# Kernel optimization log

Hardware: AMD Instinct MI355X
Metric: run time of the kernel (lower is better)

The kernel has to match this reference:

```python
import jax, jax.numpy as jnp
import numpy as np

S, B, D, H, L = 512, 512, 300, 256, 3

def setup_inputs() -> dict:
    key = jax.random.key(0)
    ks = jax.random.split(key, 9)
    sc = 0.02
    return {
        "x": jax.random.normal(ks[0], (S, B, D), dtype=jnp.float32),
        "fW_ih0": jax.random.normal(ks[1], (D, H), dtype=jnp.float32) * sc,
        "fW_ih": jax.random.normal(ks[2], (L - 1, H, H), dtype=jnp.float32) * sc,
        "fW_hh": jax.random.normal(ks[3], (L, H, H), dtype=jnp.float32) * sc,
        "fb": jnp.zeros((L, H), dtype=jnp.float32),
        "bW_ih0": jax.random.normal(ks[4], (D, H), dtype=jnp.float32) * sc,
        "bW_ih": jax.random.normal(ks[5], (L - 1, H, H), dtype=jnp.float32) * sc,
        "bW_hh": jax.random.normal(ks[6], (L, H, H), dtype=jnp.float32) * sc,
        "bb": jnp.zeros((L, H), dtype=jnp.float32),
    }

def _run_rnn(x, W_ih0, W_ih, W_hh, b):
    # x: [S, B, D]; stacked vanilla tanh RNN with L layers.
    batch = x.shape[1]
    h0 = jnp.zeros((L, batch, H), dtype=x.dtype)

    def step(h, x_t):  # h: [L, B, H], x_t: [B, D]
        inp = x_t
        new_h = []
        for l in range(L):
            Wih = W_ih0 if l == 0 else W_ih[l - 1]
            hl = jnp.tanh(inp @ Wih + h[l] @ W_hh[l] + b[l])
            new_h.append(hl)
            inp = hl
        return jnp.stack(new_h, axis=0), None

    h_final, _ = jax.lax.scan(step, h0, x)
    return h_final  # [L, B, H]

def reference(x, fW_ih0, fW_ih, fW_hh, fb, bW_ih0, bW_ih, bW_hh, bb):
    hf = _run_rnn(x, fW_ih0, fW_ih, fW_hh, fb)          # forward direction
    hb = _run_rnn(x[::-1], bW_ih0, bW_ih, bW_hh, bb)    # backward direction
    return jnp.concatenate((hf[-1], hb[-1]), axis=-1)   # [B, 2H]
```

## Files before the change

kernel.cpp:

```cpp
#include <hip/hip_runtime.h>
#include <cstdint>
#include <cstddef>


#define SEQ   512
#define BATCH 512
#define DIN   300
#define HDIM  256
#define NT    512
#define CH    64
#define NCH   (SEQ / CH)
#define NSLOT (NCH + 2)
#define TS    16
#define ZTILE 131072

typedef _Float16 f16x8 __attribute__((ext_vector_type(8)));
typedef __fp16   fp16x2 __attribute__((ext_vector_type(2)));
typedef float    f32x4 __attribute__((ext_vector_type(4)));

#define WIH0_E 0
#define WHH_E  163840
#define WIHN_E 557056
#define HC_BYTE   1638400
#define HB_BYTE   3211264
#define Z0_BYTE   (HB_BYTE + 67108864)
#define Z1_BYTE   (Z0_BYTE + 268435456)
#define Z2_BYTE   (Z1_BYTE + 67108864)
#define RING_E    8388608ull

static __device__ __forceinline__ uint16_t f16bits(_Float16 h) {
    union { _Float16 h; uint16_t u; } v; v.h = h; return v.u;
}
static __device__ __forceinline__ uint32_t pk2(float a, float b) {
    union { fp16x2 h; uint32_t u; } v; v.h = __builtin_amdgcn_cvt_pkrtz(a, b); return v.u;
}
static __device__ __forceinline__ int swz(int row, int col) {
    return (row * 256 + col) ^ ((row & 7) << 3);
}

static __device__ __forceinline__ void aload8(f16x8 r[8], const _Float16* p, size_t stepE) {
    const _Float16* p0 = p;
    const _Float16* p1 = p + stepE;
    const _Float16* p2 = p + 2 * stepE;
    const _Float16* p3 = p + 3 * stepE;
    const _Float16* p4 = p + 4 * stepE;
    const _Float16* p5 = p + 5 * stepE;
    const _Float16* p6 = p + 6 * stepE;
    const _Float16* p7 = p + 7 * stepE;
    asm volatile(
        "global_load_dwordx4 %0, %8, off\n\t"
        "global_load_dwordx4 %1, %9, off\n\t"
        "global_load_dwordx4 %2, %10, off\n\t"
        "global_load_dwordx4 %3, %11, off\n\t"
        "global_load_dwordx4 %4, %12, off\n\t"
        "global_load_dwordx4 %5, %13, off\n\t"
        "global_load_dwordx4 %6, %14, off\n\t"
        "global_load_dwordx4 %7, %15, off\n\t"
        "s_waitcnt vmcnt(0)"
        : "=&v"(r[0]), "=&v"(r[1]), "=&v"(r[2]), "=&v"(r[3]),
          "=&v"(r[4]), "=&v"(r[5]), "=&v"(r[6]), "=&v"(r[7])
        : "v"(p0), "v"(p1), "v"(p2), "v"(p3), "v"(p4), "v"(p5), "v"(p6), "v"(p7)
        : "memory");
}

__global__ void rnn_prep(const float* __restrict__ fW_ih0, const float* __restrict__ fW_ih,
                         const float* __restrict__ fW_hh,  const float* __restrict__ bW_ih0,
                         const float* __restrict__ bW_ih,  const float* __restrict__ bW_hh,
                         _Float16* __restrict__ wf)
{
    const int gid = blockIdx.x * 256 + threadIdx.x;
    const int d = gid / 51200;
    const int r = gid - d * 51200;
    const int lane = r & 63;
    const float* Wih0 = d ? bW_ih0 : fW_ih0;
    const float* Wih  = d ? bW_ih  : fW_ih;
    const float* Whh  = d ? bW_hh  : fW_hh;
    _Float16 vals[8];
    size_t dstE;
    if (r < 10240) {
        const int ck = r >> 6, ct = ck / 10, kt = ck - ct * 10;
        const int col = ct * 16 + (lane & 15);
        const int k0  = kt * 32 + (lane >> 4) * 8;
        #pragma unroll
        for (int e = 0; e < 8; ++e) {
            const int k = k0 + e;
            vals[e] = (k < 300) ? (_Float16)Wih0[(size_t)k * 256 + col] : (_Float16)0.f;
        }
        dstE = (size_t)WIH0_E + (size_t)d * 81920 + (size_t)r * 8;
    } else if (r < 34816) {
        const int rr = r - 10240, l = rr / 8192, r2 = rr - l * 8192;
        const int ck = r2 >> 6, ct = ck >> 3, kt = ck & 7;
        const int col = ct * 16 + (lane & 15);
        const int k0  = kt * 32 + (lane >> 4) * 8;
        #pragma unroll
        for (int e = 0; e < 8; ++e)
            vals[e] = (_Float16)Whh[((size_t)(l * 256 + k0 + e)) * 256 + col];
        dstE = (size_t)WHH_E + (size_t)(d * 3 + l) * 65536 + (size_t)r2 * 8;
    } else {
        const int rr = r - 34816, ln = rr / 8192, r2 = rr - ln * 8192;
        const int ck = r2 >> 6, ct = ck >> 3, kt = ck & 7;
        const int col = ct * 16 + (lane & 15);
        const int k0  = kt * 32 + (lane >> 4) * 8;
        #pragma unroll
        for (int e = 0; e < 8; ++e)
            vals[e] = (_Float16)Wih[((size_t)(ln * 256 + k0 + e)) * 256 + col];
        dstE = (size_t)WIHN_E + (size_t)(d * 2 + ln) * 65536 + (size_t)r2 * 8;
    }
    *(f16x8*)(wf + dstE) = *(const f16x8*)vals;
}

__global__ __attribute__((amdgpu_flat_work_group_size(NT, NT)))
void rnn_gemm0(const float* __restrict__ x, const _Float16* __restrict__ wih0,
               const float* __restrict__ fb, const float* __restrict__ bb,
               uint16_t* __restrict__ z0)
{
    __shared__ uint16_t Xl[2][16 * 332];
    const int tid = threadIdx.x, lane = tid & 63, w = tid >> 6;
    const int colw = lane & 15, rq = lane >> 4, rq8 = rq * 8;
    const int ct0 = w * 2;
    const int sg = blockIdx.x >> 5, rb = blockIdx.x & 31;
    const int b0 = rb * 16;
    const size_t chunk = ((size_t)(rb * 8 + w) * 64 + lane) * 8;

    int rs[5], cc2[5]; bool pv[5];
    #pragma unroll
    for (int b = 0; b < 5; ++b) {
        const int p = tid + b * NT;
        pv[b] = p < 2400;
        const int r = p / 150;
        rs[b] = r; cc2[b] = (p - r * 150) * 2;
    }

    float bv[2][2];
    #pragma unroll
    for (int dd = 0; dd < 2; ++dd)
        #pragma unroll
        for (int c = 0; c < 2; ++c)
            bv[dd][c] = (dd ? bb : fb)[(ct0 + c) * 16 + colw];

    for (int p = tid; p < 320; p += NT) {
        const int bu = p / 160, q = p - bu * 160;
        const int r = q / 10, cc = 300 + (q - r * 10) * 2;
        *(uint32_t*)&Xl[bu][r * 332 + cc] = 0;
    }
    {
        const float* xs = x + ((size_t)(sg * TS) * BATCH + b0) * DIN;
        #pragma unroll
        for (int b = 0; b < 5; ++b) if (pv[b]) {
            const float2 v = *(const float2*)(xs + (size_t)rs[b] * DIN + cc2[b]);
            *(uint32_t*)&Xl[0][rs[b] * 332 + cc2[b]] = pk2(v.x, v.y);
        }
    }
    __syncthreads();

    #pragma unroll 1
    for (int si = 0; si < TS; ++si) {
        const int s = sg * TS + si;
        const int buf = si & 1;
        const bool last = (si == TS - 1);

        {
            f32x4 a0 = (f32x4){bv[0][0], bv[0][0], bv[0][0], bv[0][0]};
            f32x4 a1 = (f32x4){bv[0][1], bv[0][1], bv[0][1], bv[0][1]};
            #pragma unroll
            for (int kt = 0; kt < 10; ++kt) {
                const f16x8 wv0 = *(const f16x8*)(wih0 + (((size_t)ct0 * 10 + kt) * 64 + lane) * 8);
                const f16x8 wv1 = *(const f16x8*)(wih0 + (((size_t)(ct0 + 1) * 10 + kt) * 64 + lane) * 8);
                const f16x8 a = *(const f16x8*)&Xl[buf][colw * 332 + kt * 32 + rq8];
                a0 = __builtin_amdgcn_mfma_f32_16x16x32_f16(a, wv0, a0, 0, 0, 0);
                a1 = __builtin_amdgcn_mfma_f32_16x16x32_f16(a, wv1, a1, 0, 0, 0);
            }
            uint4 sv;
            sv.x = pk2(a0[0], a0[1]); sv.y = pk2(a0[2], a0[3]);
            sv.z = pk2(a1[0], a1[1]); sv.w = pk2(a1[2], a1[3]);
            *(uint4*)(z0 + (size_t)s * ZTILE + chunk) = sv;
        }

        float2 xr[5];
        if (!last) {
            const float* xs = x + ((size_t)(s + 1) * BATCH + b0) * DIN;
            #pragma unroll
            for (int b = 0; b < 5; ++b) if (pv[b])
                xr[b] = *(const float2*)(xs + (size_t)rs[b] * DIN + cc2[b]);
        }

        f32x4 a0 = (f32x4){bv[1][0], bv[1][0], bv[1][0], bv[1][0]};
        f32x4 a1 = (f32x4){bv[1][1], bv[1][1], bv[1][1], bv[1][1]};
        #pragma unroll
        for (int kt = 0; kt < 10; ++kt) {
            const f16x8 wv0 = *(const f16x8*)(wih0 + 81920 + (((size_t)ct0 * 10 + kt) * 64 + lane) * 8);
            const f16x8 wv1 = *(const f16x8*)(wih0 + 81920 + (((size_t)(ct0 + 1) * 10 + kt) * 64 + lane) * 8);
            const f16x8 a = *(const f16x8*)&Xl[buf][colw * 332 + kt * 32 + rq8];
            a0 = __builtin_amdgcn_mfma_f32_16x16x32_f16(a, wv0, a0, 0, 0, 0);
            a1 = __builtin_amdgcn_mfma_f32_16x16x32_f16(a, wv1, a1, 0, 0, 0);
        }

        if (!last) {
            #pragma unroll
            for (int b = 0; b < 5; ++b) if (pv[b])
                *(uint32_t*)&Xl[buf ^ 1][rs[b] * 332 + cc2[b]] = pk2(xr[b].x, xr[b].y);
        }

        {
            uint4 sv;
            sv.x = pk2(a0[0], a0[1]); sv.y = pk2(a0[2], a0[3]);
            sv.z = pk2(a1[0], a1[1]); sv.w = pk2(a1[2], a1[3]);
            *(uint4*)(z0 + ((size_t)SEQ + (SEQ - 1 - s)) * ZTILE + chunk) = sv;
        }

        __builtin_amdgcn_sched_barrier(0);
        asm volatile("s_waitcnt lgkmcnt(0)" ::: "memory");
        __builtin_amdgcn_s_barrier();
        __builtin_amdgcn_sched_barrier(0);
    }
}

template<int L>
__device__ __forceinline__ void rec_run(const _Float16* whh_all, const _Float16* wihn_all,
                                        const uint16_t* zsrc, uint16_t* zdst,
                                        uint16_t* hcarry, const float* fb, const float* bb,
                                        float* out, int d, int i, int cs, uint16_t* Hb)
{
    const int tid = threadIdx.x, lane = tid & 63, w = tid >> 6;
    const int colw = lane & 15, rq = lane >> 4, rq8 = rq * 8;
    const int ct0 = w * 2;
    const int grow0 = i * 16;

    const _Float16* whh = whh_all + (size_t)(d * 3 + L) * 65536;
    f16x8 wh0[8], wh1[8];
    aload8(wh0, whh + ((size_t)ct0 * 8 * 64 + lane) * 8, 512);
    aload8(wh1, whh + ((size_t)(ct0 + 1) * 8 * 64 + lane) * 8, 512);
    f16x8 wn0[8], wn1[8];
    float bn0 = 0.f, bn1 = 0.f;
    if constexpr (L < 2) {
        const _Float16* wnx = wihn_all + (size_t)(d * 2 + L) * 65536;
        aload8(wn0, wnx + ((size_t)ct0 * 8 * 64 + lane) * 8, 512);
        aload8(wn1, wnx + ((size_t)(ct0 + 1) * 8 * 64 + lane) * 8, 512);
        const float* bnx = (d ? bb : fb) + (L + 1) * HDIM;
        bn0 = bnx[ct0 * 16 + colw];
        bn1 = bnx[(ct0 + 1) * 16 + colw];
    }

    for (int p = tid; p < 4096; p += NT) ((uint32_t*)Hb)[p] = 0;
    __syncthreads();
    if (cs > 0) {
        const uint16_t* hc = hcarry + (size_t)(d * 3 + L) * 131072;
        const int row = tid >> 5, c8 = (tid & 31) * 8;
        *(uint4*)&Hb[4096 + ((row * 256 + c8) ^ ((row & 7) << 3))] =
            *(const uint4*)(hc + (size_t)(grow0 + row) * 256 + c8);
    }
    __syncthreads();

    const size_t zoff = ((size_t)(i * 8 + w) * 64 + lane) * 8;

    uint4 zc = *(const uint4*)(zsrc + zoff);
    uint4 za = *(const uint4*)(zsrc + (size_t)ZTILE + zoff);
    uint4 zb = *(const uint4*)(zsrc + 2 * (size_t)ZTILE + zoff);

    f32x4 anp0 = {}, anp1 = {};

    #pragma unroll 1
    for (int k = 0; k < CH; ++k) {
        const int cur = k & 1, prv = cur ^ 1;
        const int kp = (k + 3 < CH) ? (k + 3) : (CH - 1);
        const uint4 zd = *(const uint4*)(zsrc + (size_t)kp * ZTILE + zoff);

        f16x8 ah[8];
        #pragma unroll
        for (int kt = 0; kt < 8; ++kt)
            ah[kt] = *(const f16x8*)&Hb[(prv << 12) + swz(colw, kt * 32 + rq8)];

        f32x4 ar0, ar1;
        {
            union { uint4 u; _Float16 h[8]; } zz; zz.u = zc;
            ar0 = (f32x4){(float)zz.h[0], (float)zz.h[1], (float)zz.h[2], (float)zz.h[3]};
            ar1 = (f32x4){(float)zz.h[4], (float)zz.h[5], (float)zz.h[6], (float)zz.h[7]};
        }

        f32x4 an0, an1;
        if constexpr (L < 2) {
            an0 = (f32x4){bn0, bn0, bn0, bn0};
            an1 = (f32x4){bn1, bn1, bn1, bn1};
            #pragma unroll
            for (int kt = 0; kt < 8; ++kt) {
                ar0 = __builtin_amdgcn_mfma_f32_16x16x32_f16(ah[kt], wh0[kt], ar0, 0, 0, 0);
                ar1 = __builtin_amdgcn_mfma_f32_16x16x32_f16(ah[kt], wh1[kt], ar1, 0, 0, 0);
                an0 = __builtin_amdgcn_mfma_f32_16x16x32_f16(ah[kt], wn0[kt], an0, 0, 0, 0);
                an1 = __builtin_amdgcn_mfma_f32_16x16x32_f16(ah[kt], wn1[kt], an1, 0, 0, 0);
            }
        } else {
            f32x4 arB0 = {}, arB1 = {};
            #pragma unroll
            for (int kt = 0; kt < 4; ++kt) {
                ar0  = __builtin_amdgcn_mfma_f32_16x16x32_f16(ah[kt],     wh0[kt],     ar0,  0, 0, 0);
                ar1  = __builtin_amdgcn_mfma_f32_16x16x32_f16(ah[kt],     wh1[kt],     ar1,  0, 0, 0);
                arB0 = __builtin_amdgcn_mfma_f32_16x16x32_f16(ah[4 + kt], wh0[4 + kt], arB0, 0, 0, 0);
                arB1 = __builtin_amdgcn_mfma_f32_16x16x32_f16(ah[4 + kt], wh1[4 + kt], arB1, 0, 0, 0);
            }
            ar0 = ar0 + arB0;
            ar1 = ar1 + arB1;
        }

        if constexpr (L < 2) {
            if (k >= 2) {
                uint4 sv;
                sv.x = pk2(anp0[0], anp0[1]); sv.y = pk2(anp0[2], anp0[3]);
                sv.z = pk2(anp1[0], anp1[1]); sv.w = pk2(anp1[2], anp1[3]);
                *(uint4*)(zdst + (size_t)(k - 2) * ZTILE + zoff) = sv;
            }
        }

        float hv[8];
        #pragma unroll
        for (int q = 0; q < 8; ++q) {
            const float S = (q < 4) ? ar0[q] : ar1[q - 4];
            const float e = __builtin_amdgcn_exp2f(S * 2.885390081777927f);
            const float r = __builtin_amdgcn_rcpf(e + 1.f);
            hv[q] = __builtin_fmaf(-2.f, r, 1.f);
        }
        #pragma unroll
        for (int q = 0; q < 8; ++q) {
            const int c = q >> 2, j = q & 3;
            Hb[(cur << 12) + swz(rq * 4 + j, (ct0 + c) * 16 + colw)] = f16bits((_Float16)hv[q]);
        }
        if (L == 2 && cs == NCH - 1 && k == CH - 1) {
            #pragma unroll
            for (int q = 0; q < 8; ++q) {
                const int c = q >> 2, j = q & 3;
                out[(size_t)(grow0 + rq * 4 + j) * 512 + d * 256 + (ct0 + c) * 16 + colw] = hv[q];
            }
        }

        if constexpr (L < 2) { anp0 = an0; anp1 = an1; }
        zc = za; za = zb; zb = zd;

        __builtin_amdgcn_sched_barrier(0);
        asm volatile("s_waitcnt lgkmcnt(0)" ::: "memory");
        __builtin_amdgcn_s_barrier();
        __builtin_amdgcn_sched_barrier(0);
    }

    if constexpr (L < 2) {
        {
            uint4 sv;
            sv.x = pk2(anp0[0], anp0[1]); sv.y = pk2(anp0[2], anp0[3]);
            sv.z = pk2(anp1[0], anp1[1]); sv.w = pk2(anp1[2], anp1[3]);
            *(uint4*)(zdst + (size_t)(CH - 2) * ZTILE + zoff) = sv;
        }
        f32x4 an0 = (f32x4){bn0, bn0, bn0, bn0};
        f32x4 an1 = (f32x4){bn1, bn1, bn1, bn1};
        #pragma unroll
        for (int kt = 0; kt < 8; ++kt) {
            const f16x8 ah = *(const f16x8*)&Hb[(1 << 12) + swz(colw, kt * 32 + rq8)];
            an0 = __builtin_amdgcn_mfma_f32_16x16x32_f16(ah, wn0[kt], an0, 0, 0, 0);
            an1 = __builtin_amdgcn_mfma_f32_16x16x32_f16(ah, wn1[kt], an1, 0, 0, 0);
        }
        uint4 sv;
        sv.x = pk2(an0[0], an0[1]); sv.y = pk2(an0[2], an0[3]);
        sv.z = pk2(an1[0], an1[1]); sv.w = pk2(an1[2], an1[3]);
        *(uint4*)(zdst + (size_t)(CH - 1) * ZTILE + zoff) = sv;
    }
    {
        uint16_t* hc = hcarry + (size_t)(d * 3 + L) * 131072;
        const int row = tid >> 5, c8 = (tid & 31) * 8;
        *(uint4*)(hc + (size_t)(grow0 + row) * 256 + c8) =
            *(const uint4*)&Hb[4096 + ((row * 256 + c8) ^ ((row & 7) << 3))];
    }
}

__global__ __attribute__((amdgpu_flat_work_group_size(NT, NT), amdgpu_waves_per_eu(2)))
void rnn_rec(const _Float16* whh_all, const _Float16* wihn_all,
             uint16_t* z0, uint16_t* z1, uint16_t* z2,
             uint16_t* hcarry, const float* fb, const float* bb,
             float* out, int slot)
{
    __shared__ uint16_t Hb[2 * 4096];
    const int l = blockIdx.x >> 6, sub = blockIdx.x & 63;
    const int d = sub >> 5, i = sub & 31;
    const int cs = slot - l;
    if (cs < 0 || cs >= NCH) return;
    const size_t ringE = (size_t)((cs & 1) * 2 + d) * RING_E;
    if (l == 0) {
        const uint16_t* zs = z0 + ((size_t)d * SEQ + (size_t)cs * CH) * ZTILE;
        rec_run<0>(whh_all, wihn_all, zs, z1 + ringE, hcarry, fb, bb, out, d, i, cs, Hb);
    } else if (l == 1) {
        rec_run<1>(whh_all, wihn_all, z1 + ringE, z2 + ringE, hcarry, fb, bb, out, d, i, cs, Hb);
    } else {
        rec_run<2>(whh_all, wihn_all, z2 + ringE, nullptr, hcarry, fb, bb, out, d, i, cs, Hb);
    }
}

extern "C" void kernel_launch(void* const* d_in, const int* in_sizes, int n_in,
                              void* d_out, int out_size, void* d_ws, size_t ws_size,
                              hipStream_t stream)
{
    (void)in_sizes; (void)n_in; (void)out_size; (void)ws_size;
    const float* x      = (const float*)d_in[0];
    const float* fW_ih0 = (const float*)d_in[1];
    const float* fW_ih  = (const float*)d_in[2];
    const float* fW_hh  = (const float*)d_in[3];
    const float* fb     = (const float*)d_in[4];
    const float* bW_ih0 = (const float*)d_in[5];
    const float* bW_ih  = (const float*)d_in[6];
    const float* bW_hh  = (const float*)d_in[7];
    const float* bb     = (const float*)d_in[8];
    uint8_t* ws = (uint8_t*)d_ws;

    _Float16* wf     = (_Float16*)ws;
    uint16_t* hcarry = (uint16_t*)(ws + HC_BYTE);
    uint16_t* z0     = (uint16_t*)(ws + Z0_BYTE);
    uint16_t* z1     = (uint16_t*)(ws + Z1_BYTE);
    uint16_t* z2     = (uint16_t*)(ws + Z2_BYTE);
    const _Float16* whh  = wf + WHH_E;
    const _Float16* wihn = wf + WIHN_E;
    float* out = (float*)d_out;

    rnn_prep<<<400, 256, 0, stream>>>(fW_ih0, fW_ih, fW_hh, bW_ih0, bW_ih, bW_hh, wf);
    rnn_gemm0<<<1024, NT, 0, stream>>>(x, wf, fb, bb, z0);
    for (int s = 0; s < NSLOT; ++s)
        rnn_rec<<<192, NT, 0, stream>>>(whh, wihn, z0, z1, z2, hcarry, fb, bb, out, s);
}
```

Measured before the change: 872.9 us.

## Replace chunked per-slot launches with one persistent layer-pipelined kernel using progress flags

Drops the ten chunked launches that passed hidden state between chunks through global memory. A single launch now runs all layers at once: each layer block walks all 512 timesteps and publishes its progress through agent-scope atomic flags. Downstream layer blocks spin-wait on these flags, giving fine-grained wavefront pipelining across layers and removing launch gaps and chunk pipeline fill. This needs full-length z1/z2 buffers and relies on all 192 blocks being co-resident, and the per-step polling adds some latency.

Result: slower. 1.605 ms (+83.8%).

```diff
diff --git a/kernel.cpp b/kernel.cpp
--- a/kernel.cpp
+++ b/kernel.cpp
@@ -8,9 +8,6 @@
 #define DIN   300
 #define HDIM  256
 #define NT    512
-#define CH    64
-#define NCH   (SEQ / CH)
-#define NSLOT (NCH + 2)
 #define TS    16
 #define ZTILE 131072
 
@@ -21,12 +18,10 @@
 #define WIH0_E 0
 #define WHH_E  163840
 #define WIHN_E 557056
-#define HC_BYTE   1638400
-#define HB_BYTE   3211264
-#define Z0_BYTE   (HB_BYTE + 67108864)
+#define FLAG_BYTE 1638400
+#define Z0_BYTE   2097152
 #define Z1_BYTE   (Z0_BYTE + 268435456)
-#define Z2_BYTE   (Z1_BYTE + 67108864)
-#define RING_E    8388608ull
+#define Z2_BYTE   (Z1_BYTE + 268435456)
 
 static __device__ __forceinline__ uint16_t f16bits(_Float16 h) {
     union { _Float16 h; uint16_t u; } v; v.h = h; return v.u;
@@ -36,6 +31,13 @@
 }
 static __device__ __forceinline__ int swz(int row, int col) {
     return (row * 256 + col) ^ ((row & 7) << 3);
+}
+static __device__ __forceinline__ void est16(uint16_t* p, uint4 v) {
+    uint32_t* q = (uint32_t*)p;
+    __hip_atomic_store(q + 0, v.x, __ATOMIC_RELAXED, __HIP_MEMORY_SCOPE_AGENT);
+    __hip_atomic_store(q + 1, v.y, __ATOMIC_RELAXED, __HIP_MEMORY_SCOPE_AGENT);
+    __hip_atomic_store(q + 2, v.z, __ATOMIC_RELAXED, __HIP_MEMORY_SCOPE_AGENT);
+    __hip_atomic_store(q + 3, v.w, __ATOMIC_RELAXED, __HIP_MEMORY_SCOPE_AGENT);
 }
 
 static __device__ __forceinline__ void aload8(f16x8 r[8], const _Float16* p, size_t stepE) {
@@ -66,8 +68,12 @@
 __global__ void rnn_prep(const float* __restrict__ fW_ih0, const float* __restrict__ fW_ih,
                          const float* __restrict__ fW_hh,  const float* __restrict__ bW_ih0,
                          const float* __restrict__ bW_ih,  const float* __restrict__ bW_hh,
-                         _Float16* __restrict__ wf)
+                         _Float16* __restrict__ wf, uint32_t* __restrict__ flags)
 {
+    if (blockIdx.x == 400) {
+        if (threadIdx.x < 128) flags[threadIdx.x] = 0;
+        return;
+    }
     const int gid = blockIdx.x * 256 + threadIdx.x;
     const int d = gid / 51200;
     const int r = gid - d * 51200;
@@ -217,9 +223,9 @@
 
 template<int L>
 __device__ __forceinline__ void rec_run(const _Float16* whh_all, const _Float16* wihn_all,
-                                        const uint16_t* zsrc, uint16_t* zdst,
-                                        uint16_t* hcarry, const float* fb, const float* bb,
-                                        float* out, int d, int i, int cs, uint16_t* Hb)
+                                        const uint16_t* zsb, uint16_t* zdb,
+                                        uint32_t* prog, const float* fb, const float* bb,
+                                        float* out, int d, int i, uint16_t* Hb)
 {
     const int tid = threadIdx.x, lane = tid & 63, w = tid >> 6;
     const int colw = lane & 15, rq = lane >> 4, rq8 = rq * 8;
@@ -241,29 +247,36 @@
         bn1 = bnx[(ct0 + 1) * 16 + colw];
     }
 
+    uint32_t* myP = prog + (L * 64 + d * 32 + i);
+    const uint32_t* upP = prog + ((L - 1) * 64 + d * 32 + i);
+    uint32_t seen = 0;
+
     for (int p = tid; p < 4096; p += NT) ((uint32_t*)Hb)[p] = 0;
     __syncthreads();
-    if (cs > 0) {
-        const uint16_t* hc = hcarry + (size_t)(d * 3 + L) * 131072;
-        const int row = tid >> 5, c8 = (tid & 31) * 8;
-        *(uint4*)&Hb[4096 + ((row * 256 + c8) ^ ((row & 7) << 3))] =
-            *(const uint4*)(hc + (size_t)(grow0 + row) * 256 + c8);
-    }
-    __syncthreads();
+
+    if constexpr (L > 0) {
+        if (tid == 0) {
+            while (seen < 4u) {
+                seen = __hip_atomic_load(upP, __ATOMIC_RELAXED, __HIP_MEMORY_SCOPE_AGENT);
+                if (seen >= 4u) break;
+                __builtin_amdgcn_s_sleep(2);
+            }
+        }
+        __syncthreads();
+    }
 
     const size_t zoff = ((size_t)(i * 8 + w) * 64 + lane) * 8;
-
-    uint4 zc = *(const uint4*)(zsrc + zoff);
-    uint4 za = *(const uint4*)(zsrc + (size_t)ZTILE + zoff);
-    uint4 zb = *(const uint4*)(zsrc + 2 * (size_t)ZTILE + zoff);
+    uint4 zc = *(const uint4*)(zsb + zoff);
+    uint4 za = *(const uint4*)(zsb + (size_t)ZTILE + zoff);
+    uint4 zb = *(const uint4*)(zsb + 2 * (size_t)ZTILE + zoff);
 
     f32x4 anp0 = {}, anp1 = {};
 
     #pragma unroll 1
-    for (int k = 0; k < CH; ++k) {
-        const int cur = k & 1, prv = cur ^ 1;
-        const int kp = (k + 3 < CH) ? (k + 3) : (CH - 1);
-        const uint4 zd = *(const uint4*)(zsrc + (size_t)kp * ZTILE + zoff);
+    for (int t = 0; t < SEQ; ++t) {
+        const int cur = t & 1, prv = cur ^ 1;
+        const int kp = (t + 3 < SEQ) ? (t + 3) : (SEQ - 1);
+        const uint4 zd = *(const uint4*)(zsb + (size_t)kp * ZTILE + zoff);
 
         f16x8 ah[8];
         #pragma unroll
@@ -302,11 +315,11 @@
         }
 
         if constexpr (L < 2) {
-            if (k >= 2) {
+            if (t >= 2) {
                 uint4 sv;
                 sv.x = pk2(anp0[0], anp0[1]); sv.y = pk2(anp0[2], anp0[3]);
                 sv.z = pk2(anp1[0], anp1[1]); sv.w = pk2(anp1[2], anp1[3]);
-                *(uint4*)(zdst + (size_t)(k - 2) * ZTILE + zoff) = sv;
+                est16(zdb + (size_t)(t - 2) * ZTILE + zoff, sv);
             }
         }
 
@@ -323,7 +336,7 @@
             const int c = q >> 2, j = q & 3;
             Hb[(cur << 12) + swz(rq * 4 + j, (ct0 + c) * 16 + colw)] = f16bits((_Float16)hv[q]);
         }
-        if (L == 2 && cs == NCH - 1 && k == CH - 1) {
+        if (L == 2 && t == SEQ - 1) {
             #pragma unroll
             for (int q = 0; q < 8; ++q) {
                 const int c = q >> 2, j = q & 3;
@@ -333,6 +346,21 @@
 
         if constexpr (L < 2) { anp0 = an0; anp1 = an1; }
         zc = za; za = zb; zb = zd;
+
+        if constexpr (L < 2)
+            asm volatile("s_waitcnt vmcnt(10)" ::: "memory");
+        if (tid == 0) {
+            if (L < 2 && t >= 5)
+                __hip_atomic_store(myP, (uint32_t)(t - 4), __ATOMIC_RELAXED, __HIP_MEMORY_SCOPE_AGENT);
+            if (L > 0 && t < SEQ - 1) {
+                const uint32_t tgt = (uint32_t)((t + 5 < SEQ) ? (t + 5) : SEQ);
+                while (seen < tgt) {
+                    seen = __hip_atomic_load(upP, __ATOMIC_RELAXED, __HIP_MEMORY_SCOPE_AGENT);
+                    if (seen >= tgt) break;
+                    __builtin_amdgcn_s_sleep(1);
+                }
+            }
+        }
 
         __builtin_amdgcn_sched_barrier(0);
         asm volatile("s_waitcnt lgkmcnt(0)" ::: "memory");
@@ -345,7 +373,7 @@
             uint4 sv;
             sv.x = pk2(anp0[0], anp0[1]); sv.y = pk2(anp0[2], anp0[3]);
             sv.z = pk2(anp1[0], anp1[1]); sv.w = pk2(anp1[2], anp1[3]);
-            *(uint4*)(zdst + (size_t)(CH - 2) * ZTILE + zoff) = sv;
+            est16(zdb + (size_t)(SEQ - 2) * ZTILE + zoff, sv);
         }
         f32x4 an0 = (f32x4){bn0, bn0, bn0, bn0};
         f32x4 an1 = (f32x4){bn1, bn1, bn1, bn1};
@@ -358,36 +386,29 @@
         uint4 sv;
         sv.x = pk2(an0[0], an0[1]); sv.y = pk2(an0[2], an0[3]);
         sv.z = pk2(an1[0], an1[1]); sv.w = pk2(an1[2], an1[3]);
-        *(uint4*)(zdst + (size_t)(CH - 1) * ZTILE + zoff) = sv;
-    }
-    {
-        uint16_t* hc = hcarry + (size_t)(d * 3 + L) * 131072;
-        const int row = tid >> 5, c8 = (tid & 31) * 8;
-        *(uint4*)(hc + (size_t)(grow0 + row) * 256 + c8) =
-            *(const uint4*)&Hb[4096 + ((row * 256 + c8) ^ ((row & 7) << 3))];
+        est16(zdb + (size_t)(SEQ - 1) * ZTILE + zoff, sv);
+
+        __syncthreads();
+        if (tid == 0)
+            __hip_atomic_store(myP, (uint32_t)SEQ, __ATOMIC_RELAXED, __HIP_MEMORY_SCOPE_AGENT);
     }
 }
 
 __global__ __attribute__((amdgpu_flat_work_group_size(NT, NT), amdgpu_waves_per_eu(2)))
 void rnn_rec(const _Float16* whh_all, const _Float16* wihn_all,
-             uint16_t* z0, uint16_t* z1, uint16_t* z2,
-             uint16_t* hcarry, const float* fb, const float* bb,
-             float* out, int slot)
+             uint16_t* z0, uint16_t* z1, uint16_t* z2, uint32_t* prog,
+             const float* fb, const float* bb, float* out)
 {
     __shared__ uint16_t Hb[2 * 4096];
     const int l = blockIdx.x >> 6, sub = blockIdx.x & 63;
     const int d = sub >> 5, i = sub & 31;
-    const int cs = slot - l;
-    if (cs < 0 || cs >= NCH) return;
-    const size_t ringE = (size_t)((cs & 1) * 2 + d) * RING_E;
-    if (l == 0) {
-        const uint16_t* zs = z0 + ((size_t)d * SEQ + (size_t)cs * CH) * ZTILE;
-        rec_run<0>(whh_all, wihn_all, zs, z1 + ringE, hcarry, fb, bb, out, d, i, cs, Hb);
-    } else if (l == 1) {
-        rec_run<1>(whh_all, wihn_all, z1 + ringE, z2 + ringE, hcarry, fb, bb, out, d, i, cs, Hb);
-    } else {
-        rec_run<2>(whh_all, wihn_all, z2 + ringE, nullptr, hcarry, fb, bb, out, d, i, cs, Hb);
-    }
+    const size_t dbase = (size_t)d * SEQ * ZTILE;
+    if (l == 0)
+        rec_run<0>(whh_all, wihn_all, z0 + dbase, z1 + dbase, prog, fb, bb, out, d, i, Hb);
+    else if (l == 1)
+        rec_run<1>(whh_all, wihn_all, z1 + dbase, z2 + dbase, prog, fb, bb, out, d, i, Hb);
+    else
+        rec_run<2>(whh_all, wihn_all, z2 + dbase, nullptr, prog, fb, bb, out, d, i, Hb);
 }
 
 extern "C" void kernel_launch(void* const* d_in, const int* in_sizes, int n_in,
@@ -406,17 +427,16 @@
     const float* bb     = (const float*)d_in[8];
     uint8_t* ws = (uint8_t*)d_ws;
 
-    _Float16* wf     = (_Float16*)ws;
-    uint16_t* hcarry = (uint16_t*)(ws + HC_BYTE);
-    uint16_t* z0     = (uint16_t*)(ws + Z0_BYTE);
-    uint16_t* z1     = (uint16_t*)(ws + Z1_BYTE);
-    uint16_t* z2     = (uint16_t*)(ws + Z2_BYTE);
+    _Float16* wf   = (_Float16*)ws;
+    uint32_t* prog = (uint32_t*)(ws + FLAG_BYTE);
+    uint16_t* z0   = (uint16_t*)(ws + Z0_BYTE);
+    uint16_t* z1   = (uint16_t*)(ws + Z1_BYTE);
+    uint16_t* z2   = (uint16_t*)(ws + Z2_BYTE);
     const _Float16* whh  = wf + WHH_E;
     const _Float16* wihn = wf + WIHN_E;
     float* out = (float*)d_out;
 
-    rnn_prep<<<400, 256, 0, stream>>>(fW_ih0, fW_ih, fW_hh, bW_ih0, bW_ih, bW_hh, wf);
+    rnn_prep<<<401, 256, 0, stream>>>(fW_ih0, fW_ih, fW_hh, bW_ih0, bW_ih, bW_hh, wf, prog);
     rnn_gemm0<<<1024, NT, 0, stream>>>(x, wf, fb, bb, z0);
-    for (int s = 0; s < NSLOT; ++s)
-        rnn_rec<<<192, NT, 0, stream>>>(whh, wihn, z0, z1, z2, hcarry, fb, bb, out, s);
-}
+    rnn_rec<<<192, NT, 0, stream>>>(whh, wihn, z0, z1, z2, prog, fb, bb, out);
+}
```

## Batch two timesteps per input GEMM pass and deepen recurrence z prefetch

Applied to the files above, without the earlier changes.

The layer-0 input projection now processes two timesteps per iteration, using four LDS buffers so each weight fragment loaded from global memory feeds twice as many MFMAs and the barrier count halves. The recurrence loop is unrolled by four with a rotating four-deep register prefetch of z tiles instead of a three-deep shift chain. The vmcnt wait is moved out of the weight-load asm into a separate drain call placed after the bias loads, so those loads can overlap. The cost is more registers and LDS, which could lower occupancy or add register spills.

Measured after the change: 975.0 us. +11.7%, slower.

```diff
diff --git a/kernel.cpp b/kernel.cpp
--- a/kernel.cpp
+++ b/kernel.cpp
@@ -55,12 +55,15 @@
         "global_load_dwordx4 %4, %12, off\n\t"
         "global_load_dwordx4 %5, %13, off\n\t"
         "global_load_dwordx4 %6, %14, off\n\t"
-        "global_load_dwordx4 %7, %15, off\n\t"
-        "s_waitcnt vmcnt(0)"
+        "global_load_dwordx4 %7, %15, off"
         : "=&v"(r[0]), "=&v"(r[1]), "=&v"(r[2]), "=&v"(r[3]),
           "=&v"(r[4]), "=&v"(r[5]), "=&v"(r[6]), "=&v"(r[7])
         : "v"(p0), "v"(p1), "v"(p2), "v"(p3), "v"(p4), "v"(p5), "v"(p6), "v"(p7)
         : "memory");
+}
+static __device__ __forceinline__ void adrain() {
+    asm volatile("s_waitcnt vmcnt(0)" ::: "memory");
+    __builtin_amdgcn_sched_barrier(0);
 }
 
 __global__ void rnn_prep(const float* __restrict__ fW_ih0, const float* __restrict__ fW_ih,
@@ -114,7 +117,7 @@
                const float* __restrict__ fb, const float* __restrict__ bb,
                uint16_t* __restrict__ z0)
 {
-    __shared__ uint16_t Xl[2][16 * 332];
+    __shared__ uint16_t Xl[4][16 * 332];
     const int tid = threadIdx.x, lane = tid & 63, w = tid >> 6;
     const int colw = lane & 15, rq = lane >> 4, rq8 = rq * 8;
     const int ct0 = w * 2;
@@ -138,74 +141,99 @@
         for (int c = 0; c < 2; ++c)
             bv[dd][c] = (dd ? bb : fb)[(ct0 + c) * 16 + colw];
 
-    for (int p = tid; p < 320; p += NT) {
+    for (int p = tid; p < 640; p += NT) {
         const int bu = p / 160, q = p - bu * 160;
         const int r = q / 10, cc = 300 + (q - r * 10) * 2;
         *(uint32_t*)&Xl[bu][r * 332 + cc] = 0;
     }
-    {
-        const float* xs = x + ((size_t)(sg * TS) * BATCH + b0) * DIN;
+    #pragma unroll
+    for (int sj = 0; sj < 2; ++sj) {
+        const float* xs = x + ((size_t)(sg * TS + sj) * BATCH + b0) * DIN;
         #pragma unroll
         for (int b = 0; b < 5; ++b) if (pv[b]) {
             const float2 v = *(const float2*)(xs + (size_t)rs[b] * DIN + cc2[b]);
-            *(uint32_t*)&Xl[0][rs[b] * 332 + cc2[b]] = pk2(v.x, v.y);
+            *(uint32_t*)&Xl[sj][rs[b] * 332 + cc2[b]] = pk2(v.x, v.y);
         }
     }
     __syncthreads();
 
     #pragma unroll 1
-    for (int si = 0; si < TS; ++si) {
-        const int s = sg * TS + si;
-        const int buf = si & 1;
-        const bool last = (si == TS - 1);
+    for (int pr = 0; pr < TS / 2; ++pr) {
+        const int s0 = sg * TS + pr * 2;
+        const int pb = (pr & 1) * 2;
+        const bool last = (pr == TS / 2 - 1);
 
         {
-            f32x4 a0 = (f32x4){bv[0][0], bv[0][0], bv[0][0], bv[0][0]};
-            f32x4 a1 = (f32x4){bv[0][1], bv[0][1], bv[0][1], bv[0][1]};
+            f32x4 acc[2][2];
+            #pragma unroll
+            for (int sj = 0; sj < 2; ++sj)
+                #pragma unroll
+                for (int c = 0; c < 2; ++c)
+                    acc[sj][c] = (f32x4){bv[0][c], bv[0][c], bv[0][c], bv[0][c]};
             #pragma unroll
             for (int kt = 0; kt < 10; ++kt) {
                 const f16x8 wv0 = *(const f16x8*)(wih0 + (((size_t)ct0 * 10 + kt) * 64 + lane) * 8);
                 const f16x8 wv1 = *(const f16x8*)(wih0 + (((size_t)(ct0 + 1) * 10 + kt) * 64 + lane) * 8);
-                const f16x8 a = *(const f16x8*)&Xl[buf][colw * 332 + kt * 32 + rq8];
-                a0 = __builtin_amdgcn_mfma_f32_16x16x32_f16(a, wv0, a0, 0, 0, 0);
-                a1 = __builtin_amdgcn_mfma_f32_16x16x32_f16(a, wv1, a1, 0, 0, 0);
-            }
-            uint4 sv;
-            sv.x = pk2(a0[0], a0[1]); sv.y = pk2(a0[2], a0[3]);
-            sv.z = pk2(a1[0], a1[1]); sv.w = pk2(a1[2], a1[3]);
-            *(uint4*)(z0 + (size_t)s * ZTILE + chunk) = sv;
-        }
-
-        float2 xr[5];
+                #pragma unroll
+                for (int sj = 0; sj < 2; ++sj) {
+                    const f16x8 a = *(const f16x8*)&Xl[pb + sj][colw * 332 + kt * 32 + rq8];
+                    acc[sj][0] = __builtin_amdgcn_mfma_f32_16x16x32_f16(a, wv0, acc[sj][0], 0, 0, 0);
+                    acc[sj][1] = __builtin_amdgcn_mfma_f32_16x16x32_f16(a, wv1, acc[sj][1], 0, 0, 0);
+                }
+            }
+            #pragma unroll
+            for (int sj = 0; sj < 2; ++sj) {
+                uint4 sv;
+                sv.x = pk2(acc[sj][0][0], acc[sj][0][1]); sv.y = pk2(acc[sj][0][2], acc[sj][0][3]);
+                sv.z = pk2(acc[sj][1][0], acc[sj][1][1]); sv.w = pk2(acc[sj][1][2], acc[sj][1][3]);
+                *(uint4*)(z0 + (size_t)(s0 + sj) * ZTILE + chunk) = sv;
+            }
+        }
+
+        float2 xr[2][5];
         if (!last) {
-            const float* xs = x + ((size_t)(s + 1) * BATCH + b0) * DIN;
-            #pragma unroll
-            for (int b = 0; b < 5; ++b) if (pv[b])
-                xr[b] = *(const float2*)(xs + (size_t)rs[b] * DIN + cc2[b]);
-        }
-
-        f32x4 a0 = (f32x4){bv[1][0], bv[1][0], bv[1][0], bv[1][0]};
-        f32x4 a1 = (f32x4){bv[1][1], bv[1][1], bv[1][1], bv[1][1]};
-        #pragma unroll
-        for (int kt = 0; kt < 10; ++kt) {
-            const f16x8 wv0 = *(const f16x8*)(wih0 + 81920 + (((size_t)ct0 * 10 + kt) * 64 + lane) * 8);
-            const f16x8 wv1 = *(const f16x8*)(wih0 + 81920 + (((size_t)(ct0 + 1) * 10 + kt) * 64 + lane) * 8);
-            const f16x8 a = *(const f16x8*)&Xl[buf][colw * 332 + kt * 32 + rq8];
-            a0 = __builtin_amdgcn_mfma_f32_16x16x32_f16(a, wv0, a0, 0, 0, 0);
-            a1 = __builtin_amdgcn_mfma_f32_16x16x32_f16(a, wv1, a1, 0, 0, 0);
+            #pragma unroll
+            for (int sj = 0; sj < 2; ++sj) {
+                const float* xs = x + ((size_t)(s0 + 2 + sj) * BATCH + b0) * DIN;
+                #pragma unroll
+                for (int b = 0; b < 5; ++b) if (pv[b])
+                    xr[sj][b] = *(const float2*)(xs + (size_t)rs[b] * DIN + cc2[b]);
+            }
+        }
+
+        {
+            f32x4 acc[2][2];
+            #pragma unroll
+            for (int sj = 0; sj < 2; ++sj)
+                #pragma unroll
+                for (int c = 0; c < 2; ++c)
+                    acc[sj][c] = (f32x4){bv[1][c], bv[1][c], bv[1][c], bv[1][c]};
+            #pragma unroll
+            for (int kt = 0; kt < 10; ++kt) {
+                const f16x8 wv0 = *(const f16x8*)(wih0 + 81920 + (((size_t)ct0 * 10 + kt) * 64 + lane) * 8);
+                const f16x8 wv1 = *(const f16x8*)(wih0 + 81920 + (((size_t)(ct0 + 1) * 10 + kt) * 64 + lane) * 8);
+                #pragma unroll
+                for (int sj = 0; sj < 2; ++sj) {
+                    const f16x8 a = *(const f16x8*)&Xl[pb + sj][colw * 332 + kt * 32 + rq8];
+                    acc[sj][0] = __builtin_amdgcn_mfma_f32_16x16x32_f16(a, wv0, acc[sj][0], 0, 0, 0);
+                    acc[sj][1] = __builtin_amdgcn_mfma_f32_16x16x32_f16(a, wv1, acc[sj][1], 0, 0, 0);
+                }
+            }
+            #pragma unroll
+            for (int sj = 0; sj < 2; ++sj) {
+                uint4 sv;
+                sv.x = pk2(acc[sj][0][0], acc[sj][0][1]); sv.y = pk2(acc[sj][0][2], acc[sj][0][3]);
+                sv.z = pk2(acc[sj][1][0], acc[sj][1][1]); sv.w = pk2(acc[sj][1][2], acc[sj][1][3]);
+                *(uint4*)(z0 + ((size_t)SEQ + (SEQ - 1 - (s0 + sj))) * ZTILE + chunk) = sv;
+            }
         }
 
         if (!last) {
             #pragma unroll
-            for (int b = 0; b < 5; ++b) if (pv[b])
-                *(uint32_t*)&Xl[buf ^ 1][rs[b] * 332 + cc2[b]] = pk2(xr[b].x, xr[b].y);
-        }
-
-        {
-            uint4 sv;
-            sv.x = pk2(a0[0], a0[1]); sv.y = pk2(a0[2], a0[3]);
-            sv.z = pk2(a1[0], a1[1]); sv.w = pk2(a1[2], a1[3]);
-            *(uint4*)(z0 + ((size_t)SEQ + (SEQ - 1 - s)) * ZTILE + chunk) = sv;
+            for (int sj = 0; sj < 2; ++sj)
+                #pragma unroll
+                for (int b = 0; b < 5; ++b) if (pv[b])
+                    *(uint32_t*)&Xl[(pb ^ 2) + sj][rs[b] * 332 + cc2[b]] = pk2(xr[sj][b].x, xr[sj][b].y);
         }
 
         __builtin_amdgcn_sched_barrier(0);
@@ -240,6 +268,7 @@
         bn0 = bnx[ct0 * 16 + colw];
         bn1 = bnx[(ct0 + 1) * 16 + colw];
     }
+    adrain();
 
     for (int p = tid; p < 4096; p += NT) ((uint32_t*)Hb)[p] = 0;
     __syncthreads();
@@ -253,91 +282,97 @@
 
     const size_t zoff = ((size_t)(i * 8 + w) * 64 + lane) * 8;
 
-    uint4 zc = *(const uint4*)(zsrc + zoff);
-    uint4 za = *(const uint4*)(zsrc + (size_t)ZTILE + zoff);
-    uint4 zb = *(const uint4*)(zsrc + 2 * (size_t)ZTILE + zoff);
+    uint4 zp[4];
+    #pragma unroll
+    for (int j = 0; j < 4; ++j)
+        zp[j] = *(const uint4*)(zsrc + (size_t)j * ZTILE + zoff);
 
     f32x4 anp0 = {}, anp1 = {};
 
     #pragma unroll 1
-    for (int k = 0; k < CH; ++k) {
-        const int cur = k & 1, prv = cur ^ 1;
-        const int kp = (k + 3 < CH) ? (k + 3) : (CH - 1);
-        const uint4 zd = *(const uint4*)(zsrc + (size_t)kp * ZTILE + zoff);
-
-        f16x8 ah[8];
-        #pragma unroll
-        for (int kt = 0; kt < 8; ++kt)
-            ah[kt] = *(const f16x8*)&Hb[(prv << 12) + swz(colw, kt * 32 + rq8)];
-
-        f32x4 ar0, ar1;
-        {
-            union { uint4 u; _Float16 h[8]; } zz; zz.u = zc;
-            ar0 = (f32x4){(float)zz.h[0], (float)zz.h[1], (float)zz.h[2], (float)zz.h[3]};
-            ar1 = (f32x4){(float)zz.h[4], (float)zz.h[5], (float)zz.h[6], (float)zz.h[7]};
-        }
-
-        f32x4 an0, an1;
-        if constexpr (L < 2) {
-            an0 = (f32x4){bn0, bn0, bn0, bn0};
-            an1 = (f32x4){bn1, bn1, bn1, bn1};
-            #pragma unroll
-            for (int kt = 0; kt < 8; ++kt) {
-                ar0 = __builtin_amdgcn_mfma_f32_16x16x32_f16(ah[kt], wh0[kt], ar0, 0, 0, 0);
-                ar1 = __builtin_amdgcn_mfma_f32_16x16x32_f16(ah[kt], wh1[kt], ar1, 0, 0, 0);
-                an0 = __builtin_amdgcn_mfma_f32_16x16x32_f16(ah[kt], wn0[kt], an0, 0, 0, 0);
-                an1 = __builtin_amdgcn_mfma_f32_16x16x32_f16(ah[kt], wn1[kt], an1, 0, 0, 0);
-            }
-        } else {
-            f32x4 arB0 = {}, arB1 = {};
-            #pragma unroll
-            for (int kt = 0; kt < 4; ++kt) {
-                ar0  = __builtin_amdgcn_mfma_f32_16x16x32_f16(ah[kt],     wh0[kt],     ar0,  0, 0, 0);
-                ar1  = __builtin_amdgcn_mfma_f32_16x16x32_f16(ah[kt],     wh1[kt],     ar1,  0, 0, 0);
-                arB0 = __builtin_amdgcn_mfma_f32_16x16x32_f16(ah[4 + kt], wh0[4 + kt], arB0, 0, 0, 0);
-                arB1 = __builtin_amdgcn_mfma_f32_16x16x32_f16(ah[4 + kt], wh1[4 + kt], arB1, 0, 0, 0);
-            }
-            ar0 = ar0 + arB0;
-            ar1 = ar1 + arB1;
-        }
-
-        if constexpr (L < 2) {
-            if (k >= 2) {
-                uint4 sv;
-                sv.x = pk2(anp0[0], anp0[1]); sv.y = pk2(anp0[2], anp0[3]);
-                sv.z = pk2(anp1[0], anp1[1]); sv.w = pk2(anp1[2], anp1[3]);
-                *(uint4*)(zdst + (size_t)(k - 2) * ZTILE + zoff) = sv;
-            }
-        }
-
-        float hv[8];
-        #pragma unroll
-        for (int q = 0; q < 8; ++q) {
-            const float S = (q < 4) ? ar0[q] : ar1[q - 4];
-            const float e = __builtin_amdgcn_exp2f(S * 2.885390081777927f);
-            const float r = __builtin_amdgcn_rcpf(e + 1.f);
-            hv[q] = __builtin_fmaf(-2.f, r, 1.f);
-        }
-        #pragma unroll
-        for (int q = 0; q < 8; ++q) {
-            const int c = q >> 2, j = q & 3;
-            Hb[(cur << 12) + swz(rq * 4 + j, (ct0 + c) * 16 + colw)] = f16bits((_Float16)hv[q]);
-        }
-        if (L == 2 && cs == NCH - 1 && k == CH - 1) {
+    for (int k0 = 0; k0 < CH; k0 += 4) {
+        #pragma unroll
+        for (int u = 0; u < 4; ++u) {
+            const int k = k0 + u;
+            const int cur = u & 1, prv = cur ^ 1;
+
+            f32x4 ar0, ar1;
+            {
+                union { uint4 v; _Float16 h[8]; } zz; zz.v = zp[u];
+                ar0 = (f32x4){(float)zz.h[0], (float)zz.h[1], (float)zz.h[2], (float)zz.h[3]};
+                ar1 = (f32x4){(float)zz.h[4], (float)zz.h[5], (float)zz.h[6], (float)zz.h[7]};
+            }
+            {
+                const int kp = (k + 4 < CH) ? (k + 4) : (CH - 1);
+                zp[u] = *(const uint4*)(zsrc + (size_t)kp * ZTILE + zoff);
+            }
+
+            f16x8 ah[8];
+            #pragma unroll
+            for (int kt = 0; kt < 8; ++kt)
+                ah[kt] = *(const f16x8*)&Hb[(prv << 12) + swz(colw, kt * 32 + rq8)];
+
+            f32x4 an0, an1;
+            if constexpr (L < 2) {
+                an0 = (f32x4){bn0, bn0, bn0, bn0};
+                an1 = (f32x4){bn1, bn1, bn1, bn1};
+                #pragma unroll
+                for (int kt = 0; kt < 8; ++kt) {
+                    ar0 = __builtin_amdgcn_mfma_f32_16x16x32_f16(ah[kt], wh0[kt], ar0, 0, 0, 0);
+                    ar1 = __builtin_amdgcn_mfma_f32_16x16x32_f16(ah[kt], wh1[kt], ar1, 0, 0, 0);
+                    an0 = __builtin_amdgcn_mfma_f32_16x16x32_f16(ah[kt], wn0[kt], an0, 0, 0, 0);
+                    an1 = __builtin_amdgcn_mfma_f32_16x16x32_f16(ah[kt], wn1[kt], an1, 0, 0, 0);
+                }
+            } else {
+                f32x4 arB0 = {}, arB1 = {};
+                #pragma unroll
+                for (int kt = 0; kt < 4; ++kt) {
+                    ar0  = __builtin_amdgcn_mfma_f32_16x16x32_f16(ah[kt],     wh0[kt],     ar0,  0, 0, 0);
+                    ar1  = __builtin_amdgcn_mfma_f32_16x16x32_f16(ah[kt],     wh1[kt],     ar1,  0, 0, 0);
+                    arB0 = __builtin_amdgcn_mfma_f32_16x16x32_f16(ah[4 + kt], wh0[4 + kt], arB0, 0, 0, 0);
+                    arB1 = __builtin_amdgcn_mfma_f32_16x16x32_f16(ah[4 + kt], wh1[4 + kt], arB1, 0, 0, 0);
+                }
+                ar0 = ar0 + arB0;
+                ar1 = ar1 + arB1;
+            }
+
+            if constexpr (L < 2) {
+                if (k >= 2) {
+                    uint4 sv;
+                    sv.x = pk2(anp0[0], anp0[1]); sv.y = pk2(anp0[2], anp0[3]);
+                    sv.z = pk2(anp1[0], anp1[1]); sv.w = pk2(anp1[2], anp1[3]);
+                    *(uint4*)(zdst + (size_t)(k - 2) * ZTILE + zoff) = sv;
+                }
+            }
+
+            float hv[8];
+            #pragma unroll
+            for (int q = 0; q < 8; ++q) {
+                const float S = (q < 4) ? ar0[q] : ar1[q - 4];
+                const float e = __builtin_amdgcn_exp2f(S * 2.885390081777927f);
+                const float r = __builtin_amdgcn_rcpf(e + 1.f);
+                hv[q] = __builtin_fmaf(-2.f, r, 1.f);
+            }
             #pragma unroll
             for (int q = 0; q < 8; ++q) {
                 const int c = q >> 2, j = q & 3;
-                out[(size_t)(grow0 + rq * 4 + j) * 512 + d * 256 + (ct0 + c) * 16 + colw] = hv[q];
-            }
-        }
-
-        if constexpr (L < 2) { anp0 = an0; anp1 = an1; }
-        zc = za; za = zb; zb = zd;
-
-        __builtin_amdgcn_sched_barrier(0);
-        asm volatile("s_waitcnt lgkmcnt(0)" ::: "memory");
-        __builtin_amdgcn_s_barrier();
-        __builtin_amdgcn_sched_barrier(0);
+                Hb[(cur << 12) + swz(rq * 4 + j, (ct0 + c) * 16 + colw)] = f16bits((_Float16)hv[q]);
+            }
+            if (L == 2 && cs == NCH - 1 && k == CH - 1) {
+                #pragma unroll
+                for (int q = 0; q < 8; ++q) {
+                    const int c = q >> 2, j = q & 3;
+                    out[(size_t)(grow0 + rq * 4 + j) * 512 + d * 256 + (ct0 + c) * 16 + colw] = hv[q];
+                }
+            }
+
+            if constexpr (L < 2) { anp0 = an0; anp1 = an1; }
+
+            __builtin_amdgcn_sched_barrier(0);
+            asm volatile("s_waitcnt lgkmcnt(0)" ::: "memory");
+            __builtin_amdgcn_s_barrier();
+            __builtin_amdgcn_sched_barrier(0);
+        }
     }
 
     if constexpr (L < 2) {
```
